# Performance work log

Measured on AMD Instinct MI355X. Metric: run time of the kernel, lower is better.

Reference implementation:

```python
import jax, jax.numpy as jnp
import numpy as np

BS, SEQ, D, H, NK = 4, 256, 256, 8, 16


def _ln(x, g, b, eps=1e-5):
    m = x.mean(-1, keepdims=True)
    v = ((x - m) ** 2).mean(-1, keepdims=True)
    return (x - m) / jnp.sqrt(v + eps) * g + b


def _attention(q, k, v, mask, gammas, maxout):
    # q,k,v: [b,h,s,dk]; mask: [1,1,s,s] bool; gammas: [h,1,1]
    dk = q.shape[-1]
    scores = jnp.einsum('bhqd,bhkd->bhqk', q, k) / jnp.sqrt(jnp.asarray(dk, q.dtype))
    seqlen = scores.shape[-1]
    ar = jnp.arange(seqlen)
    pos = jnp.abs(ar[None, :] - ar[:, None]).astype(scores.dtype)[None, None]
    # distance-decay term (computed under no_grad in the original)
    s_ = jax.nn.softmax(jnp.where(mask, scores, -1e32), axis=-1)
    distcum = jnp.cumsum(s_, axis=-1)
    disttotal = jnp.sum(s_, axis=-1, keepdims=True)
    dist = jax.lax.stop_gradient(jnp.sqrt(jnp.clip((disttotal - distcum) * pos, 0.0, None)))
    g = -jnp.abs(gammas)[None]  # [1,h,1,1]
    effect = jnp.clip(jnp.exp(dist * g), 1e-5, 1e5)
    scores = scores * effect
    scores = jax.nn.softmax(jnp.where(mask, scores, -1e32), axis=-1)
    scores = jnp.where(mask, scores, 0.0)
    if maxout:
        scale = jnp.minimum(1.0 / (jnp.max(scores, axis=-1, keepdims=True) + 1e-8), 5.0)
        scores = scores * scale
    return jnp.einsum('bhqk,bhkd->bhqd', scores, v), scores


def _mha(xq, xk, xv, Wq, bq, Wk, bk, Wv, bv, Wo, bo, gammas, mask, maxout):
    bs, seq, d = xq.shape
    h = gammas.shape[0]
    dk = d // h
    def heads(x, W, b):
        return (x @ W + b).reshape(bs, seq, h, dk).transpose(0, 2, 1, 3)
    o, sc = _attention(heads(xq, Wq, bq), heads(xk, Wk, bk), heads(xv, Wv, bv), mask, gammas, maxout)
    o = o.transpose(0, 2, 1, 3).reshape(bs, seq, d)
    return o @ Wo + bo, sc


def _block(xq, xk, xv, Wq, bq, Wk, bk, Wv, bv, Wo, bo, gammas, lng, lnb, peek_cur):
    seq = xq.shape[1]
    mask = jnp.tril(jnp.ones((seq, seq), bool), 0 if peek_cur else -1)[None, None]
    out, sc = _mha(xq, xk, xv, Wq, bq, Wk, bk, Wv, bv, Wo, bo, gammas, mask, not peek_cur)
    return _ln(xq + out, lng, lnb), sc


def _dtransformer(q_emb, s_emb, know_params,
                  Wq1, bq1, Wv1, bv1, Wo1, bo1, gam1, lng1, lnb1,
                  Wq2, bq2, Wv2, bv2, Wo2, bo2, gam2, lng2, lnb2,
                  Wq3, bq3, Wv3, bv3, Wo3, bo3, gam3, lng3, lnb3,
                  Wq4, bq4, Wk4, bk4, Wv4, bv4, Wo4, bo4, gam4, lng4, lnb4):
    # n_blocks == 3 path; kq_same=True for blocks 1-3 (Wk := Wq)
    hq, _ = _block(q_emb, q_emb, q_emb, Wq1, bq1, Wq1, bq1, Wv1, bv1, Wo1, bo1, gam1, lng1, lnb1, True)
    hs, _ = _block(s_emb, s_emb, s_emb, Wq2, bq2, Wq2, bq2, Wv2, bv2, Wo2, bo2, gam2, lng2, lnb2, True)
    p, q_scores = _block(hq, hq, hs, Wq3, bq3, Wq3, bq3, Wv3, bv3, Wo3, bo3, gam3, lng3, lnb3, True)
    bs, seq, d = p.shape
    nk = know_params.shape[0]
    query = jnp.broadcast_to(know_params[None, :, None, :], (bs, nk, seq, d)).reshape(bs * nk, seq, d)
    hq_r = jnp.broadcast_to(hq[:, None], (bs, nk, seq, d)).reshape(bs * nk, seq, d)
    p_r = jnp.broadcast_to(p[:, None], (bs, nk, seq, d)).reshape(bs * nk, seq, d)
    z, k_sc = _block(query, hq_r, p_r, Wq4, bq4, Wk4, bk4, Wv4, bv4, Wo4, bo4, gam4, lng4, lnb4, False)
    z = z.reshape(bs, nk, seq, d).transpose(0, 2, 1, 3).reshape(bs, seq, nk * d)
    h = gam4.shape[0]
    k_scores = k_sc.reshape(bs, nk, h, seq, seq).transpose(0, 2, 3, 1, 4)
    return z, q_scores, k_scores


_PARAM_NAMES = []
for _b in ('1', '2', '3', '4'):
    _PARAM_NAMES += ['Wq' + _b, 'bq' + _b]
    if _b == '4':
        _PARAM_NAMES += ['Wk4', 'bk4']
    _PARAM_NAMES += ['Wv' + _b, 'bv' + _b, 'Wo' + _b, 'bo' + _b, 'gam' + _b, 'lng' + _b, 'lnb' + _b]


def setup_inputs() -> dict:
    key = jax.random.key(0)
    ks = jax.random.split(key, 64)
    inp = {}
    inp['q_emb'] = jax.random.normal(ks[0], (BS, SEQ, D), jnp.float32)
    inp['s_emb'] = jax.random.normal(ks[1], (BS, SEQ, D), jnp.float32)
    inp['lens'] = jax.random.randint(ks[2], (BS,), 1, SEQ)
    inp['know_params'] = jax.random.uniform(ks[3], (NK, D), jnp.float32, -1.0, 1.0)
    i = 4
    for name in _PARAM_NAMES:
        if name.startswith('W'):
            inp[name] = jax.random.normal(ks[i], (D, D), jnp.float32) * 0.02; i += 1
        elif name.startswith('b'):
            inp[name] = jnp.zeros((D,), jnp.float32)
        elif name.startswith('gam'):
            inp[name] = jax.random.normal(ks[i], (H, 1, 1), jnp.float32) * 0.3; i += 1
        elif name.startswith('lng'):
            inp[name] = jnp.ones((D,), jnp.float32)
        else:
            inp[name] = jnp.zeros((D,), jnp.float32)
    return inp


def reference(q_emb, s_emb, lens, know_params,
              Wq1, bq1, Wv1, bv1, Wo1, bo1, gam1, lng1, lnb1,
              Wq2, bq2, Wv2, bv2, Wo2, bo2, gam2, lng2, lnb2,
              Wq3, bq3, Wv3, bv3, Wo3, bo3, gam3, lng3, lnb3,
              Wq4, bq4, Wk4, bk4, Wv4, bv4, Wo4, bo4, gam4, lng4, lnb4):
    return _dtransformer(q_emb, s_emb, know_params,
                         Wq1, bq1, Wv1, bv1, Wo1, bo1, gam1, lng1, lnb1,
                         Wq2, bq2, Wv2, bv2, Wo2, bo2, gam2, lng2, lnb2,
                         Wq3, bq3, Wv3, bv3, Wo3, bo3, gam3, lng3, lnb3,
                         Wq4, bq4, Wk4, bk4, Wv4, bv4, Wo4, bo4, gam4, lng4, lnb4)
```

## Files before the change

kernel.cpp:

```cpp
#include <hip/hip_runtime.h>
#include <math.h>

#define SEQL 256
#define DM   256
#define NH   8
#define DKH  32
#define BSZ  4
#define NKN  16

__device__ __forceinline__ float wave_red_sum(float v) {
#pragma unroll
  for (int o = 32; o > 0; o >>= 1) v += __shfl_xor(v, o);
  return v;
}
__device__ __forceinline__ float wave_red_max(float v) {
#pragma unroll
  for (int o = 32; o > 0; o >>= 1) v = fmaxf(v, __shfl_xor(v, o));
  return v;
}
__device__ __forceinline__ float wave_incl_scan(float v) {
  const int lane = threadIdx.x & 63;
#pragma unroll
  for (int o = 1; o < 64; o <<= 1) {
    float u = __shfl_up(v, o);
    if (lane >= o) v += u;
  }
  return v;
}

struct GemmSet { const float* A; const float* W; const float* bias; float* C; int M; };
struct Gemm4 { GemmSet s[4]; };

__global__ __launch_bounds__(256) void dt_gemmN(Gemm4 args) {
  const GemmSet g = args.s[blockIdx.z];
  const int bm = blockIdx.x * 64, bn = blockIdx.y * 64;
  if (bm >= g.M) return;
  __shared__ float As[16][68];
  __shared__ float Bs[16][68];
  const int tid = threadIdx.x;
  const int tc = tid & 15, tr = tid >> 4;
  float acc[4][4] = {};
  for (int k0 = 0; k0 < DM; k0 += 16) {
    {
      const int m = tid >> 2, kq = tid & 3;
      int row = bm + m; row = row < g.M ? row : (g.M - 1);
      const float4 v = *reinterpret_cast<const float4*>(&g.A[(size_t)row * DM + k0 + kq * 4]);
      As[kq * 4 + 0][m] = v.x; As[kq * 4 + 1][m] = v.y;
      As[kq * 4 + 2][m] = v.z; As[kq * 4 + 3][m] = v.w;
    }
    {
      const int k = tid >> 4, nq = tid & 15;
      const float4 v = *reinterpret_cast<const float4*>(&g.W[(size_t)(k0 + k) * DM + bn + nq * 4]);
      *reinterpret_cast<float4*>(&Bs[k][nq * 4]) = v;
    }
    __syncthreads();
#pragma unroll
    for (int k = 0; k < 16; ++k) {
      float a[4], b[4];
#pragma unroll
      for (int i = 0; i < 4; ++i) a[i] = As[k][tr * 4 + i];
#pragma unroll
      for (int j = 0; j < 4; ++j) b[j] = Bs[k][tc * 4 + j];
#pragma unroll
      for (int i = 0; i < 4; ++i)
#pragma unroll
        for (int j = 0; j < 4; ++j) acc[i][j] = fmaf(a[i], b[j], acc[i][j]);
    }
    __syncthreads();
  }
#pragma unroll
  for (int i = 0; i < 4; ++i) {
    const int row = bm + tr * 4 + i;
    if (row >= g.M) continue;
    float4 o;
    o.x = acc[i][0] + g.bias[bn + tc * 4 + 0];
    o.y = acc[i][1] + g.bias[bn + tc * 4 + 1];
    o.z = acc[i][2] + g.bias[bn + tc * 4 + 2];
    o.w = acc[i][3] + g.bias[bn + tc * 4 + 3];
    *reinterpret_cast<float4*>(&g.C[(size_t)row * DM + bn + tc * 4]) = o;
  }
}

__global__ __launch_bounds__(256) void dt_scores_nt2(const float* __restrict__ Q0,
                                                     const float* __restrict__ Q1,
                                                     float* __restrict__ Sa,
                                                     float* __restrict__ Sb) {
  const int z = blockIdx.z;
  const int set = z >> 5, bh = z & 31;
  const float* Qp = set ? Q1 : Q0;
  float* S = set ? Sb : Sa;
  const int b = bh >> 3, h = bh & 7;
  const float* Q = Qp + (size_t)b * SEQL * DM + h * DKH;
  __shared__ float Qs[16][33], Ks[16][33];
  const int tid = threadIdx.x;
  const int tj = tid & 15, ti = tid >> 4;
  const int i0 = blockIdx.x * 16, j0 = blockIdx.y * 16;
  const int r = tid >> 5, c = tid & 31;
  Qs[r][c]     = Q[(size_t)(i0 + r) * DM + c];
  Qs[r + 8][c] = Q[(size_t)(i0 + 8 + r) * DM + c];
  Ks[r][c]     = Q[(size_t)(j0 + r) * DM + c];
  Ks[r + 8][c] = Q[(size_t)(j0 + 8 + r) * DM + c];
  __syncthreads();
  float acc = 0.f;
#pragma unroll
  for (int k = 0; k < DKH; ++k) acc = fmaf(Qs[ti][k], Ks[tj][k], acc);
  S[((size_t)bh * SEQL + i0 + ti) * SEQL + j0 + tj] = acc * 0.17677669529663687f;
}

__global__ __launch_bounds__(256) void dt_scores4(const float* __restrict__ Q4h,
                                                  const float* __restrict__ Kp,
                                                  float* __restrict__ S0) {
  const int idx = blockIdx.x * 256 + threadIdx.x;
  const int j = idx & 255;
  const int h = (idx >> 8) & 7;
  const int nk = (idx >> 11) & 15;
  const int b = idx >> 15;
  const float* q = Q4h + nk * DM + h * DKH;
  const float* k = Kp + ((size_t)(b * SEQL + j)) * DM + h * DKH;
  float acc = 0.f;
#pragma unroll
  for (int c = 0; c < DKH; ++c) acc = fmaf(q[c], k[c], acc);
  S0[idx] = acc * 0.17677669529663687f;
}

__global__ __launch_bounds__(256) void dt_prep4(const float* __restrict__ S0,
                                                float* __restrict__ Pfx) {
  const int wid = threadIdx.x >> 6, lane = threadIdx.x & 63;
  const int row = blockIdx.x * 4 + wid;
  const float4 s4 = *reinterpret_cast<const float4*>(S0 + (size_t)row * SEQL + lane * 4);
  float s[4] = {s4.x, s4.y, s4.z, s4.w};
  float mx = fmaxf(fmaxf(s[0], s[1]), fmaxf(s[2], s[3]));
  mx = wave_red_max(mx);
  float e[4], t = 0.f;
#pragma unroll
  for (int q = 0; q < 4; ++q) { e[q] = __expf(s[q] - mx); t += e[q]; }
  const float incl = wave_incl_scan(t);
  float run = incl - t;
  float4 o;
  run += e[0]; o.x = run;
  run += e[1]; o.y = run;
  run += e[2]; o.z = run;
  run += e[3]; o.w = run;
  *reinterpret_cast<float4*>(Pfx + (size_t)row * SEQL + lane * 4) = o;
}

__global__ __launch_bounds__(256) void dt_softmax13w2(const float* __restrict__ Sa,
                                                      const float* __restrict__ Sb,
                                                      float* __restrict__ Pa,
                                                      float* __restrict__ Pb,
                                                      const float* __restrict__ g0,
                                                      const float* __restrict__ g1) {
  const int wid = threadIdx.x >> 6, lane = threadIdx.x & 63;
  const int grow = blockIdx.x * 4 + wid;
  const int set = grow >> 13;
  const int row = grow & 8191;
  const float* S = set ? Sb : Sa;
  float* P = set ? Pb : Pa;
  const float* gam = set ? g1 : g0;
  const int i = row & 255, h = (row >> 8) & 7;
  const float g = -fabsf(gam[h]);
  const int jb = lane * 4;
  const float4 s4 = *reinterpret_cast<const float4*>(S + (size_t)row * SEQL + jb);
  float s[4] = {s4.x, s4.y, s4.z, s4.w};
  float mx = -1e30f;
#pragma unroll
  for (int q = 0; q < 4; ++q) if (jb + q <= i) mx = fmaxf(mx, s[q]);
  mx = wave_red_max(mx);
  float e[4], t = 0.f;
#pragma unroll
  for (int q = 0; q < 4; ++q) { e[q] = (jb + q <= i) ? __expf(s[q] - mx) : 0.f; t += e[q]; }
  const float incl = wave_incl_scan(t);
  const float total = __shfl(incl, 63);
  const float inv = 1.f / total;
  float run = incl - t;
  float p2[4], t2 = 0.f;
#pragma unroll
  for (int q = 0; q < 4; ++q) {
    run += e[q];
    const float cum = run * inv;
    float dd = (1.f - cum) * (float)(i - jb - q);
    dd = dd > 0.f ? dd : 0.f;
    float eff = __expf(g * sqrtf(dd));
    eff = fmaxf(eff, 1e-5f);
    const float y = s[q] * eff;
    p2[q] = (jb + q <= i) ? __expf(y) : 0.f;
    t2 += p2[q];
  }
  const float sum2 = wave_red_sum(t2);
  const float inv2 = 1.f / sum2;
  float4 o = {p2[0] * inv2, p2[1] * inv2, p2[2] * inv2, p2[3] * inv2};
  *reinterpret_cast<float4*>(P + (size_t)row * SEQL + jb) = o;
}

__global__ __launch_bounds__(256) void dt_sm_pv4(const float* __restrict__ S0,
                                                 const float* __restrict__ Pfx,
                                                 const float* __restrict__ Vp,
                                                 const float* __restrict__ gam,
                                                 float* __restrict__ KS,
                                                 float* __restrict__ O) {
  __shared__ float Vs[256][32];
  __shared__ float Pl[32][268];
  __shared__ float Pfl[256];
  const int z = blockIdx.x;
  const int h = z & 7, b = z >> 7;
  const int nk = (z >> 3) & 15, bnk = z >> 3;
  const int tid = threadIdx.x, lane = tid & 63, w = tid >> 6;
  const float* Vbase = Vp + (size_t)b * SEQL * DM + h * DKH;
  {
    const int j = tid >> 3, c4 = (tid & 7) * 4;
    for (int jj = 0; jj < 256; jj += 32) {
      const float4 v = *reinterpret_cast<const float4*>(Vbase + (size_t)(jj + j) * DM + c4);
      *reinterpret_cast<float4*>(&Vs[jj + j][c4]) = v;
    }
  }
  if (tid < 64) {
    const float4 p = *reinterpret_cast<const float4*>(Pfx + (size_t)z * SEQL + tid * 4);
    *reinterpret_cast<float4*>(&Pfl[tid * 4]) = p;
  }
  const float4 s4 = *reinterpret_cast<const float4*>(S0 + (size_t)z * SEQL + lane * 4);
  const float4 p4 = *reinterpret_cast<const float4*>(Pfx + (size_t)z * SEQL + lane * 4);
  const float s[4] = {s4.x, s4.y, s4.z, s4.w};
  const float pj[4] = {p4.x, p4.y, p4.z, p4.w};
  const float g = -fabsf(gam[h]);
  const int jb = lane * 4;
  const int r0 = tid >> 5, cg = tid & 7, jq = (tid >> 3) & 3;
  __syncthreads();

  for (int chunk = 0; chunk < 8; ++chunk) {
    const int i0 = chunk * 32;
#pragma unroll
    for (int r = 0; r < 8; ++r) {
      const int il = w * 8 + r;
      const int i = i0 + il;
      float pv[4];
      if (i == 0) {
        pv[0] = pv[1] = pv[2] = pv[3] = 0.f;
      } else {
        const float rinv = 1.f / Pfl[i - 1];
        float t = 0.f, m = 0.f;
#pragma unroll
        for (int q = 0; q < 4; ++q) {
          const float cum = pj[q] * rinv;
          float dd = (1.f - cum) * (float)(i - jb - q);
          dd = dd > 0.f ? dd : 0.f;
          float eff = __expf(g * sqrtf(dd));
          eff = fmaxf(eff, 1e-5f);
          const float y = s[q] * eff;
          pv[q] = (jb + q < i) ? __expf(y) : 0.f;
          t += pv[q];
          m = fmaxf(m, pv[q]);
        }
#pragma unroll
        for (int o = 32; o > 0; o >>= 1) {
          t += __shfl_xor(t, o);
          m = fmaxf(m, __shfl_xor(m, o));
        }
        const float inv2 = 1.f / t;
        const float scale = fminf(1.f / (m * inv2 + 1e-8f), 5.f);
        const float f = inv2 * scale;
        pv[0] *= f; pv[1] *= f; pv[2] *= f; pv[3] *= f;
      }
      const float4 o4 = {pv[0], pv[1], pv[2], pv[3]};
      *reinterpret_cast<float4*>(KS + ((((size_t)(b * NH + h)) * SEQL + i) * NKN + nk) * SEQL + jb) = o4;
      *reinterpret_cast<float4*>(&Pl[il][jb]) = o4;
    }
    __syncthreads();
    float4 acc[4] = {{0.f,0.f,0.f,0.f},{0.f,0.f,0.f,0.f},{0.f,0.f,0.f,0.f},{0.f,0.f,0.f,0.f}};
#pragma unroll 4
    for (int t4 = 0; t4 < 16; ++t4) {
      const int jb2 = t4 * 16 + jq * 4;
      float pr[4][4];
#pragma unroll
      for (int r = 0; r < 4; ++r) {
        const float4 p = *reinterpret_cast<const float4*>(&Pl[r0 * 4 + r][jb2]);
        pr[r][0] = p.x; pr[r][1] = p.y; pr[r][2] = p.z; pr[r][3] = p.w;
      }
#pragma unroll
      for (int k = 0; k < 4; ++k) {
        const float4 v = *reinterpret_cast<const float4*>(&Vs[jb2 + k][cg * 4]);
#pragma unroll
        for (int r = 0; r < 4; ++r) {
          acc[r].x = fmaf(pr[r][k], v.x, acc[r].x);
          acc[r].y = fmaf(pr[r][k], v.y, acc[r].y);
          acc[r].z = fmaf(pr[r][k], v.z, acc[r].z);
          acc[r].w = fmaf(pr[r][k], v.w, acc[r].w);
        }
      }
    }
#pragma unroll
    for (int r = 0; r < 4; ++r) {
      acc[r].x += __shfl_xor(acc[r].x, 8);  acc[r].x += __shfl_xor(acc[r].x, 16);
      acc[r].y += __shfl_xor(acc[r].y, 8);  acc[r].y += __shfl_xor(acc[r].y, 16);
      acc[r].z += __shfl_xor(acc[r].z, 8);  acc[r].z += __shfl_xor(acc[r].z, 16);
      acc[r].w += __shfl_xor(acc[r].w, 8);  acc[r].w += __shfl_xor(acc[r].w, 16);
    }
    if ((tid & 24) == 0) {
#pragma unroll
      for (int r = 0; r < 4; ++r)
        *reinterpret_cast<float4*>(O + ((size_t)(bnk * SEQL + i0 + r0 * 4 + r)) * DM + h * DKH + cg * 4) = acc[r];
    }
    __syncthreads();
  }
}

__global__ __launch_bounds__(256) void dt_pv13_2(const float* __restrict__ Pa,
                                                 const float* __restrict__ Pb,
                                                 const float* __restrict__ V0,
                                                 const float* __restrict__ V1,
                                                 float* __restrict__ Oa,
                                                 float* __restrict__ Ob) {
  __shared__ float Vs[256][32];
  __shared__ float Pl[32][268];
  const int z = blockIdx.y;
  const int set = z >> 5, bh = z & 31;
  const float* P = set ? Pb : Pa;
  const float* Vp = set ? V1 : V0;
  float* O = set ? Ob : Oa;
  const int b = bh >> 3, h = bh & 7;
  const int i0 = blockIdx.x * 32;
  const int tid = threadIdx.x;
  const float* Prow = P + ((size_t)bh * SEQL + i0) * SEQL;
  const float* Vbase = Vp + (size_t)b * SEQL * DM + h * DKH;
#pragma unroll
  for (int t = 0; t < 8; ++t) {
    const int idx = t * 256 + tid;
    const int j = idx >> 3, c4 = (idx & 7) * 4;
    *reinterpret_cast<float4*>(&Vs[j][c4]) =
        *reinterpret_cast<const float4*>(Vbase + (size_t)j * DM + c4);
    const int prw = idx >> 6, pc4 = (idx & 63) * 4;
    *reinterpret_cast<float4*>(&Pl[prw][pc4]) =
        *reinterpret_cast<const float4*>(Prow + (size_t)prw * SEQL + pc4);
  }
  __syncthreads();
  const int r0 = tid >> 5, cg = tid & 7, jq = (tid >> 3) & 3;
  float4 acc[4] = {{0.f,0.f,0.f,0.f},{0.f,0.f,0.f,0.f},{0.f,0.f,0.f,0.f},{0.f,0.f,0.f,0.f}};
#pragma unroll 4
  for (int t4 = 0; t4 < 16; ++t4) {
    const int jb2 = t4 * 16 + jq * 4;
    float pr[4][4];
#pragma unroll
    for (int r = 0; r < 4; ++r) {
      const float4 p = *reinterpret_cast<const float4*>(&Pl[r0 * 4 + r][jb2]);
      pr[r][0] = p.x; pr[r][1] = p.y; pr[r][2] = p.z; pr[r][3] = p.w;
    }
#pragma unroll
    for (int k = 0; k < 4; ++k) {
      const float4 v = *reinterpret_cast<const float4*>(&Vs[jb2 + k][cg * 4]);
#pragma unroll
      for (int r = 0; r < 4; ++r) {
        acc[r].x = fmaf(pr[r][k], v.x, acc[r].x);
        acc[r].y = fmaf(pr[r][k], v.y, acc[r].y);
        acc[r].z = fmaf(pr[r][k], v.z, acc[r].z);
        acc[r].w = fmaf(pr[r][k], v.w, acc[r].w);
      }
    }
  }
#pragma unroll
  for (int r = 0; r < 4; ++r) {
    acc[r].x += __shfl_xor(acc[r].x, 8);  acc[r].x += __shfl_xor(acc[r].x, 16);
    acc[r].y += __shfl_xor(acc[r].y, 8);  acc[r].y += __shfl_xor(acc[r].y, 16);
    acc[r].z += __shfl_xor(acc[r].z, 8);  acc[r].z += __shfl_xor(acc[r].z, 16);
    acc[r].w += __shfl_xor(acc[r].w, 8);  acc[r].w += __shfl_xor(acc[r].w, 16);
  }
  if ((tid & 24) == 0) {
#pragma unroll
    for (int r = 0; r < 4; ++r)
      *reinterpret_cast<float4*>(O + ((size_t)(b * SEQL + i0 + r0 * 4 + r)) * DM + h * DKH + cg * 4) = acc[r];
  }
}

__global__ __launch_bounds__(256) void dt_ln_res2(const float* __restrict__ X0,
                                                  const float* __restrict__ X1,
                                                  const float* __restrict__ Y0,
                                                  const float* __restrict__ Y1,
                                                  const float* __restrict__ G0,
                                                  const float* __restrict__ G1,
                                                  const float* __restrict__ B0,
                                                  const float* __restrict__ B1,
                                                  float* __restrict__ Z0,
                                                  float* __restrict__ Z1) {
  const int wid = threadIdx.x >> 6, lane = threadIdx.x & 63;
  const int grow = blockIdx.x * 4 + wid;
  const int set = grow >> 10;
  const int row = grow & 1023;
  const float* X = set ? X1 : X0;
  const float* Y = set ? Y1 : Y0;
  const float* g = set ? G1 : G0;
  const float* bb = set ? B1 : B0;
  float* Z = set ? Z1 : Z0;
  const int jb = lane * 4;
  const float4 x4 = *reinterpret_cast<const float4*>(X + (size_t)row * DM + jb);
  const float4 y4 = *reinterpret_cast<const float4*>(Y + (size_t)row * DM + jb);
  float x[4] = {x4.x + y4.x, x4.y + y4.y, x4.z + y4.z, x4.w + y4.w};
  const float mean = wave_red_sum(x[0] + x[1] + x[2] + x[3]) * (1.f / 256.f);
  float vs = 0.f;
#pragma unroll
  for (int q = 0; q < 4; ++q) { const float d = x[q] - mean; vs += d * d; }
  const float var = wave_red_sum(vs) * (1.f / 256.f);
  const float rstd = 1.f / sqrtf(var + 1e-5f);
  const float4 g4 = *reinterpret_cast<const float4*>(g + jb);
  const float4 b4 = *reinterpret_cast<const float4*>(bb + jb);
  float4 o;
  o.x = (x[0] - mean) * rstd * g4.x + b4.x;
  o.y = (x[1] - mean) * rstd * g4.y + b4.y;
  o.z = (x[2] - mean) * rstd * g4.z + b4.z;
  o.w = (x[3] - mean) * rstd * g4.w + b4.w;
  *reinterpret_cast<float4*>(Z + (size_t)row * DM + jb) = o;
}

__global__ __launch_bounds__(256) void dt_ln4w(const float* __restrict__ know,
                                               const float* __restrict__ Y,
                                               const float* __restrict__ g,
                                               const float* __restrict__ bb,
                                               float* __restrict__ Z) {
  const int wid = threadIdx.x >> 6, lane = threadIdx.x & 63;
  const int row = blockIdx.x * 4 + wid;
  const int i = row & 255;
  const int nk = (row >> 8) & 15;
  const int b = row >> 12;
  const int jb = lane * 4;
  const float4 k4 = *reinterpret_cast<const float4*>(know + (size_t)nk * DM + jb);
  const float4 y4 = *reinterpret_cast<const float4*>(Y + (size_t)row * DM + jb);
  float x[4] = {k4.x + y4.x, k4.y + y4.y, k4.z + y4.z, k4.w + y4.w};
  const float mean = wave_red_sum(x[0] + x[1] + x[2] + x[3]) * (1.f / 256.f);
  float vs = 0.f;
#pragma unroll
  for (int q = 0; q < 4; ++q) { const float d = x[q] - mean; vs += d * d; }
  const float var = wave_red_sum(vs) * (1.f / 256.f);
  const float rstd = 1.f / sqrtf(var + 1e-5f);
  const float4 g4 = *reinterpret_cast<const float4*>(g + jb);
  const float4 b4 = *reinterpret_cast<const float4*>(bb + jb);
  float4 o;
  o.x = (x[0] - mean) * rstd * g4.x + b4.x;
  o.y = (x[1] - mean) * rstd * g4.y + b4.y;
  o.z = (x[2] - mean) * rstd * g4.z + b4.z;
  o.w = (x[3] - mean) * rstd * g4.w + b4.w;
  *reinterpret_cast<float4*>(Z + ((size_t)(b * SEQL + i)) * (NKN * DM) + (size_t)nk * DM + jb) = o;
}

extern "C" void kernel_launch(void* const* d_in, const int* in_sizes, int n_in,
                              void* d_out, int out_size, void* d_ws, size_t ws_size,
                              hipStream_t stream) {
  (void)in_sizes; (void)n_in; (void)out_size; (void)ws_size;
  const float* q_emb = (const float*)d_in[0];
  const float* s_emb = (const float*)d_in[1];
  const float* know  = (const float*)d_in[3];
  const float* Wq1 = (const float*)d_in[4],  *bq1 = (const float*)d_in[5];
  const float* Wv1 = (const float*)d_in[6],  *bv1 = (const float*)d_in[7];
  const float* Wo1 = (const float*)d_in[8],  *bo1 = (const float*)d_in[9];
  const float* gam1 = (const float*)d_in[10], *lng1 = (const float*)d_in[11], *lnb1 = (const float*)d_in[12];
  const float* Wq2 = (const float*)d_in[13], *bq2 = (const float*)d_in[14];
  const float* Wv2 = (const float*)d_in[15], *bv2 = (const float*)d_in[16];
  const float* Wo2 = (const float*)d_in[17], *bo2 = (const float*)d_in[18];
  const float* gam2 = (const float*)d_in[19], *lng2 = (const float*)d_in[20], *lnb2 = (const float*)d_in[21];
  const float* Wq3 = (const float*)d_in[22], *bq3 = (const float*)d_in[23];
  const float* Wv3 = (const float*)d_in[24], *bv3 = (const float*)d_in[25];
  const float* Wo3 = (const float*)d_in[26], *bo3 = (const float*)d_in[27];
  const float* gam3 = (const float*)d_in[28], *lng3 = (const float*)d_in[29], *lnb3 = (const float*)d_in[30];
  const float* Wq4 = (const float*)d_in[31], *bq4 = (const float*)d_in[32];
  const float* Wk4 = (const float*)d_in[33], *bk4 = (const float*)d_in[34];
  const float* Wv4 = (const float*)d_in[35], *bv4 = (const float*)d_in[36];
  const float* Wo4 = (const float*)d_in[37], *bo4 = (const float*)d_in[38];
  const float* gam4 = (const float*)d_in[39], *lng4 = (const float*)d_in[40], *lnb4 = (const float*)d_in[41];

  float* ws = (float*)d_ws;
  const size_t U = 262144;
  float* Qp0 = ws + 0 * U;
  float* Qp1 = ws + 1 * U;
  float* Vp0 = ws + 2 * U;
  float* Vp1 = ws + 3 * U;
  float* Sa  = ws + 4 * U;
  float* Sb  = ws + 12 * U;
  float* O0  = ws + 20 * U;
  float* O1  = ws + 21 * U;
  float* OW0 = ws + 22 * U;
  float* OW1 = ws + 23 * U;
  float* hq  = ws + 24 * U;
  float* hs  = ws + 25 * U;
  float* pbf = ws + 26 * U;
  float* Q4h = ws + 27 * U;
  float* S0s = Q4h + 4096;
  float* OW4 = Sa;
  float* Pfx = O0;

  float* zout = (float*)d_out;
  float* qsc  = zout + 4194304;
  float* ksc  = qsc + 2097152;
  float* O4   = zout;

  const dim3 thr(256);

  {
    Gemm4 a = {{{q_emb, Wq1, bq1, Qp0, 1024}, {q_emb, Wv1, bv1, Vp0, 1024},
                {s_emb, Wq2, bq2, Qp1, 1024}, {s_emb, Wv2, bv2, Vp1, 1024}}};
    dt_gemmN<<<dim3(16, 4, 4), thr, 0, stream>>>(a);
  }
  dt_scores_nt2<<<dim3(16, 16, 64), thr, 0, stream>>>(Qp0, Qp1, Sa, Sb);
  dt_softmax13w2<<<dim3(4096), thr, 0, stream>>>(Sa, Sb, Sa, Sb, gam1, gam2);
  dt_pv13_2<<<dim3(8, 64), thr, 0, stream>>>(Sa, Sb, Vp0, Vp1, O0, O1);
  {
    Gemm4 a = {{{O0, Wo1, bo1, OW0, 1024}, {O1, Wo2, bo2, OW1, 1024},
                {O0, Wo1, bo1, OW0, 1024}, {O1, Wo2, bo2, OW1, 1024}}};
    dt_gemmN<<<dim3(16, 4, 2), thr, 0, stream>>>(a);
  }
  dt_ln_res2<<<dim3(512), thr, 0, stream>>>(q_emb, s_emb, OW0, OW1, lng1, lng2, lnb1, lnb2, hq, hs);

  {
    Gemm4 a = {{{hq, Wq3, bq3, Qp0, 1024}, {hs, Wv3, bv3, Vp0, 1024},
                {hq, Wq3, bq3, Qp0, 1024}, {hs, Wv3, bv3, Vp0, 1024}}};
    dt_gemmN<<<dim3(16, 4, 2), thr, 0, stream>>>(a);
  }
  dt_scores_nt2<<<dim3(16, 16, 32), thr, 0, stream>>>(Qp0, Qp0, Sa, Sa);
  dt_softmax13w2<<<dim3(2048), thr, 0, stream>>>(Sa, Sa, qsc, qsc, gam3, gam3);
  dt_pv13_2<<<dim3(8, 32), thr, 0, stream>>>(qsc, qsc, Vp0, Vp0, O0, O0);
  {
    Gemm4 a = {{{O0, Wo3, bo3, OW0, 1024}, {O0, Wo3, bo3, OW0, 1024},
                {O0, Wo3, bo3, OW0, 1024}, {O0, Wo3, bo3, OW0, 1024}}};
    dt_gemmN<<<dim3(16, 4, 1), thr, 0, stream>>>(a);
  }
  dt_ln_res2<<<dim3(256), thr, 0, stream>>>(hq, hq, OW0, OW0, lng3, lng3, lnb3, lnb3, pbf, pbf);

  {
    Gemm4 a = {{{hq, Wk4, bk4, Qp0, 1024}, {pbf, Wv4, bv4, Vp0, 1024},
                {know, Wq4, bq4, Q4h, 16}, {know, Wq4, bq4, Q4h, 16}}};
    dt_gemmN<<<dim3(16, 4, 3), thr, 0, stream>>>(a);
  }
  dt_scores4<<<dim3(512), thr, 0, stream>>>(Q4h, Qp0, S0s);
  dt_prep4<<<dim3(128), thr, 0, stream>>>(S0s, Pfx);
  dt_sm_pv4<<<dim3(512), thr, 0, stream>>>(S0s, Pfx, Vp0, gam4, ksc, O4);
  {
    Gemm4 a = {{{O4, Wo4, bo4, OW4, 16384}, {O4, Wo4, bo4, OW4, 16384},
                {O4, Wo4, bo4, OW4, 16384}, {O4, Wo4, bo4, OW4, 16384}}};
    dt_gemmN<<<dim3(256, 4, 1), thr, 0, stream>>>(a);
  }
  dt_ln4w<<<dim3(4096), thr, 0, stream>>>(know, OW4, lng4, lnb4, zout);
}
```

Before: 516.1 us.

## Use bf16 LDS tiles for PV, split sm_pv4 rows, retile scores and small GEMMs

The P·V kernels now store P and a transposed V in LDS as bf16 and unpack them to fp32 for the FMAs. This halves LDS footprint and read traffic, and they get launch bounds allowing four blocks per CU. dt_sm_pv4 splits its eight row chunks across two blocks to double parallelism, at the cost of each block reloading V. The scores kernel moves to 32x32 tiles with four outputs per thread and float4 loads, and the 1024-row GEMMs use a new 32-row tile kernel for more blocks. Rounding P and V to bf16 lowers the precision of the attention output.

```diff
diff --git a/kernel.cpp b/kernel.cpp
--- a/kernel.cpp
+++ b/kernel.cpp
@@ -7,6 +7,7 @@
 #define DKH  32
 #define BSZ  4
 #define NKN  16
+#define LSTR 264
 
 __device__ __forceinline__ float wave_red_sum(float v) {
 #pragma unroll
@@ -26,6 +27,62 @@
     if (lane >= o) v += u;
   }
   return v;
+}
+
+__device__ __forceinline__ unsigned short bf16r(float f) {
+  unsigned u = __float_as_uint(f);
+  u = (u + 0x7fffu + ((u >> 16) & 1u)) >> 16;
+  return (unsigned short)u;
+}
+__device__ __forceinline__ unsigned pack_bf16x2(float a, float b) {
+  return (unsigned)bf16r(a) | ((unsigned)bf16r(b) << 16);
+}
+
+__device__ __forceinline__ void pv_core(const unsigned short (*Pl)[LSTR],
+                                        const unsigned short (*Vt)[LSTR],
+                                        int tid, float acc[4][4]) {
+  const int r0 = tid >> 5, cg = tid & 7, jq = (tid >> 3) & 3;
+#pragma unroll
+  for (int t = 0; t < 8; ++t) {
+    const int j0 = t * 32 + jq * 8;
+    uint4 pu[4], vu[4];
+#pragma unroll
+    for (int r = 0; r < 4; ++r) pu[r] = *reinterpret_cast<const uint4*>(&Pl[r0 * 4 + r][j0]);
+#pragma unroll
+    for (int c = 0; c < 4; ++c) vu[c] = *reinterpret_cast<const uint4*>(&Vt[cg * 4 + c][j0]);
+#pragma unroll
+    for (int d = 0; d < 4; ++d) {
+      float pl[4], ph[4], vl[4], vh[4];
+#pragma unroll
+      for (int r = 0; r < 4; ++r) {
+        const unsigned w = (&pu[r].x)[d];
+        pl[r] = __uint_as_float(w << 16);
+        ph[r] = __uint_as_float(w & 0xffff0000u);
+      }
+#pragma unroll
+      for (int c = 0; c < 4; ++c) {
+        const unsigned w = (&vu[c].x)[d];
+        vl[c] = __uint_as_float(w << 16);
+        vh[c] = __uint_as_float(w & 0xffff0000u);
+      }
+#pragma unroll
+      for (int r = 0; r < 4; ++r)
+#pragma unroll
+        for (int c = 0; c < 4; ++c)
+          acc[r][c] = fmaf(ph[r], vh[c], fmaf(pl[r], vl[c], acc[r][c]));
+    }
+  }
+}
+__device__ __forceinline__ void pv_reduce_jq(int tid, float acc[4][4]) {
+#pragma unroll
+  for (int r = 0; r < 4; ++r)
+#pragma unroll
+    for (int c = 0; c < 4; ++c) {
+      float v = acc[r][c];
+      v += __shfl_xor(v, 8);
+      v += __shfl_xor(v, 16);
+      acc[r][c] = v;
+    }
 }
 
 struct GemmSet { const float* A; const float* W; const float* bias; float* C; int M; };
@@ -81,6 +138,53 @@
   }
 }
 
+__global__ __launch_bounds__(256) void dt_gemm32(Gemm4 args) {
+  const GemmSet g = args.s[blockIdx.z];
+  const int bm = blockIdx.x * 32, bn = blockIdx.y * 64;
+  __shared__ float As[16][36];
+  __shared__ float Bs[16][68];
+  const int tid = threadIdx.x;
+  const int tc = tid & 15, tr = tid >> 4;
+  float acc[2][4] = {};
+  for (int k0 = 0; k0 < DM; k0 += 16) {
+    if (tid < 128) {
+      const int m = tid >> 2, kq = tid & 3;
+      const float4 v = *reinterpret_cast<const float4*>(&g.A[(size_t)(bm + m) * DM + k0 + kq * 4]);
+      As[kq * 4 + 0][m] = v.x; As[kq * 4 + 1][m] = v.y;
+      As[kq * 4 + 2][m] = v.z; As[kq * 4 + 3][m] = v.w;
+    }
+    {
+      const int k = tid >> 4, nq = tid & 15;
+      const float4 v = *reinterpret_cast<const float4*>(&g.W[(size_t)(k0 + k) * DM + bn + nq * 4]);
+      *reinterpret_cast<float4*>(&Bs[k][nq * 4]) = v;
+    }
+    __syncthreads();
+#pragma unroll
+    for (int k = 0; k < 16; ++k) {
+      float a[2], b[4];
+      a[0] = As[k][tr * 2 + 0];
+      a[1] = As[k][tr * 2 + 1];
+#pragma unroll
+      for (int j = 0; j < 4; ++j) b[j] = Bs[k][tc * 4 + j];
+#pragma unroll
+      for (int i = 0; i < 2; ++i)
+#pragma unroll
+        for (int j = 0; j < 4; ++j) acc[i][j] = fmaf(a[i], b[j], acc[i][j]);
+    }
+    __syncthreads();
+  }
+#pragma unroll
+  for (int i = 0; i < 2; ++i) {
+    const int row = bm + tr * 2 + i;
+    float4 o;
+    o.x = acc[i][0] + g.bias[bn + tc * 4 + 0];
+    o.y = acc[i][1] + g.bias[bn + tc * 4 + 1];
+    o.z = acc[i][2] + g.bias[bn + tc * 4 + 2];
+    o.w = acc[i][3] + g.bias[bn + tc * 4 + 3];
+    *reinterpret_cast<float4*>(&g.C[(size_t)row * DM + bn + tc * 4]) = o;
+  }
+}
+
 __global__ __launch_bounds__(256) void dt_scores_nt2(const float* __restrict__ Q0,
                                                      const float* __restrict__ Q1,
                                                      float* __restrict__ Sa,
@@ -91,20 +195,28 @@
   float* S = set ? Sb : Sa;
   const int b = bh >> 3, h = bh & 7;
   const float* Q = Qp + (size_t)b * SEQL * DM + h * DKH;
-  __shared__ float Qs[16][33], Ks[16][33];
+  __shared__ float Qs[32][33], Ks[32][33];
   const int tid = threadIdx.x;
-  const int tj = tid & 15, ti = tid >> 4;
-  const int i0 = blockIdx.x * 16, j0 = blockIdx.y * 16;
-  const int r = tid >> 5, c = tid & 31;
-  Qs[r][c]     = Q[(size_t)(i0 + r) * DM + c];
-  Qs[r + 8][c] = Q[(size_t)(i0 + 8 + r) * DM + c];
-  Ks[r][c]     = Q[(size_t)(j0 + r) * DM + c];
-  Ks[r + 8][c] = Q[(size_t)(j0 + 8 + r) * DM + c];
+  const int i0 = blockIdx.x * 32, j0 = blockIdx.y * 32;
+  {
+    const int r = tid >> 3, gq = (tid & 7) * 4;
+    const float4 q = *reinterpret_cast<const float4*>(&Q[(size_t)(i0 + r) * DM + gq]);
+    Qs[r][gq + 0] = q.x; Qs[r][gq + 1] = q.y; Qs[r][gq + 2] = q.z; Qs[r][gq + 3] = q.w;
+    const float4 k = *reinterpret_cast<const float4*>(&Q[(size_t)(j0 + r) * DM + gq]);
+    Ks[r][gq + 0] = k.x; Ks[r][gq + 1] = k.y; Ks[r][gq + 2] = k.z; Ks[r][gq + 3] = k.w;
+  }
   __syncthreads();
-  float acc = 0.f;
-#pragma unroll
-  for (int k = 0; k < DKH; ++k) acc = fmaf(Qs[ti][k], Ks[tj][k], acc);
-  S[((size_t)bh * SEQL + i0 + ti) * SEQL + j0 + tj] = acc * 0.17677669529663687f;
+  const int tj = tid & 31, tig = tid >> 5;
+  float acc[4] = {0.f, 0.f, 0.f, 0.f};
+#pragma unroll
+  for (int k = 0; k < DKH; ++k) {
+    const float bk = Ks[tj][k];
+#pragma unroll
+    for (int r = 0; r < 4; ++r) acc[r] = fmaf(Qs[tig * 4 + r][k], bk, acc[r]);
+  }
+#pragma unroll
+  for (int r = 0; r < 4; ++r)
+    S[((size_t)bh * SEQL + i0 + tig * 4 + r) * SEQL + j0 + tj] = acc[r] * 0.17677669529663687f;
 }
 
 __global__ __launch_bounds__(256) void dt_scores4(const float* __restrict__ Q4h,
@@ -192,25 +304,30 @@
   *reinterpret_cast<float4*>(P + (size_t)row * SEQL + jb) = o;
 }
 
-__global__ __launch_bounds__(256) void dt_sm_pv4(const float* __restrict__ S0,
-                                                 const float* __restrict__ Pfx,
-                                                 const float* __restrict__ Vp,
-                                                 const float* __restrict__ gam,
-                                                 float* __restrict__ KS,
-                                                 float* __restrict__ O) {
-  __shared__ float Vs[256][32];
-  __shared__ float Pl[32][268];
+__global__ __launch_bounds__(256, 4) void dt_sm_pv4(const float* __restrict__ S0,
+                                                    const float* __restrict__ Pfx,
+                                                    const float* __restrict__ Vp,
+                                                    const float* __restrict__ gam,
+                                                    float* __restrict__ KS,
+                                                    float* __restrict__ O) {
+  __shared__ unsigned short Vt[32][LSTR];
+  __shared__ unsigned short Pl[32][LSTR];
   __shared__ float Pfl[256];
-  const int z = blockIdx.x;
+  const int z = blockIdx.y;
   const int h = z & 7, b = z >> 7;
   const int nk = (z >> 3) & 15, bnk = z >> 3;
   const int tid = threadIdx.x, lane = tid & 63, w = tid >> 6;
   const float* Vbase = Vp + (size_t)b * SEQL * DM + h * DKH;
   {
-    const int j = tid >> 3, c4 = (tid & 7) * 4;
-    for (int jj = 0; jj < 256; jj += 32) {
-      const float4 v = *reinterpret_cast<const float4*>(Vbase + (size_t)(jj + j) * DM + c4);
-      *reinterpret_cast<float4*>(&Vs[jj + j][c4]) = v;
+    const int jr = tid >> 3, gq = tid & 7;
+#pragma unroll
+    for (int t = 0; t < 8; ++t) {
+      const int j = jr + t * 32;
+      const float4 v = *reinterpret_cast<const float4*>(Vbase + (size_t)j * DM + gq * 4);
+      Vt[gq * 4 + 0][j] = bf16r(v.x);
+      Vt[gq * 4 + 1][j] = bf16r(v.y);
+      Vt[gq * 4 + 2][j] = bf16r(v.z);
+      Vt[gq * 4 + 3][j] = bf16r(v.w);
     }
   }
   if (tid < 64) {
@@ -223,10 +340,10 @@
   const float pj[4] = {p4.x, p4.y, p4.z, p4.w};
   const float g = -fabsf(gam[h]);
   const int jb = lane * 4;
-  const int r0 = tid >> 5, cg = tid & 7, jq = (tid >> 3) & 3;
+  const int r0 = tid >> 5, cg = tid & 7;
   __syncthreads();
 
-  for (int chunk = 0; chunk < 8; ++chunk) {
+  for (int chunk = blockIdx.x * 4; chunk < blockIdx.x * 4 + 4; ++chunk) {
     const int i0 = chunk * 32;
 #pragma unroll
     for (int r = 0; r < 8; ++r) {
@@ -262,55 +379,32 @@
       }
       const float4 o4 = {pv[0], pv[1], pv[2], pv[3]};
       *reinterpret_cast<float4*>(KS + ((((size_t)(b * NH + h)) * SEQL + i) * NKN + nk) * SEQL + jb) = o4;
-      *reinterpret_cast<float4*>(&Pl[il][jb]) = o4;
+      uint2 pk = {pack_bf16x2(pv[0], pv[1]), pack_bf16x2(pv[2], pv[3])};
+      *reinterpret_cast<uint2*>(&Pl[il][jb]) = pk;
     }
     __syncthreads();
-    float4 acc[4] = {{0.f,0.f,0.f,0.f},{0.f,0.f,0.f,0.f},{0.f,0.f,0.f,0.f},{0.f,0.f,0.f,0.f}};
-#pragma unroll 4
-    for (int t4 = 0; t4 < 16; ++t4) {
-      const int jb2 = t4 * 16 + jq * 4;
-      float pr[4][4];
+    float acc[4][4] = {};
+    pv_core(Pl, Vt, tid, acc);
+    pv_reduce_jq(tid, acc);
+    if ((tid & 24) == 0) {
 #pragma unroll
       for (int r = 0; r < 4; ++r) {
-        const float4 p = *reinterpret_cast<const float4*>(&Pl[r0 * 4 + r][jb2]);
-        pr[r][0] = p.x; pr[r][1] = p.y; pr[r][2] = p.z; pr[r][3] = p.w;
+        const float4 oo = {acc[r][0], acc[r][1], acc[r][2], acc[r][3]};
+        *reinterpret_cast<float4*>(O + ((size_t)(bnk * SEQL + i0 + r0 * 4 + r)) * DM + h * DKH + cg * 4) = oo;
       }
-#pragma unroll
-      for (int k = 0; k < 4; ++k) {
-        const float4 v = *reinterpret_cast<const float4*>(&Vs[jb2 + k][cg * 4]);
-#pragma unroll
-        for (int r = 0; r < 4; ++r) {
-          acc[r].x = fmaf(pr[r][k], v.x, acc[r].x);
-          acc[r].y = fmaf(pr[r][k], v.y, acc[r].y);
-          acc[r].z = fmaf(pr[r][k], v.z, acc[r].z);
-          acc[r].w = fmaf(pr[r][k], v.w, acc[r].w);
-        }
-      }
-    }
-#pragma unroll
-    for (int r = 0; r < 4; ++r) {
-      acc[r].x += __shfl_xor(acc[r].x, 8);  acc[r].x += __shfl_xor(acc[r].x, 16);
-      acc[r].y += __shfl_xor(acc[r].y, 8);  acc[r].y += __shfl_xor(acc[r].y, 16);
-      acc[r].z += __shfl_xor(acc[r].z, 8);  acc[r].z += __shfl_xor(acc[r].z, 16);
-      acc[r].w += __shfl_xor(acc[r].w, 8);  acc[r].w += __shfl_xor(acc[r].w, 16);
-    }
-    if ((tid & 24) == 0) {
-#pragma unroll
-      for (int r = 0; r < 4; ++r)
-        *reinterpret_cast<float4*>(O + ((size_t)(bnk * SEQL + i0 + r0 * 4 + r)) * DM + h * DKH + cg * 4) = acc[r];
     }
     __syncthreads();
   }
 }
 
-__global__ __launch_bounds__(256) void dt_pv13_2(const float* __restrict__ Pa,
-                                                 const float* __restrict__ Pb,
-                                                 const float* __restrict__ V0,
-                                                 const float* __restrict__ V1,
-                                                 float* __restrict__ Oa,
-                                                 float* __restrict__ Ob) {
-  __shared__ float Vs[256][32];
-  __shared__ float Pl[32][268];
+__global__ __launch_bounds__(256, 4) void dt_pv13_2(const float* __restrict__ Pa,
+                                                    const float* __restrict__ Pb,
+                                                    const float* __restrict__ V0,
+                                                    const float* __restrict__ V1,
+                                                    float* __restrict__ Oa,
+                                                    float* __restrict__ Ob) {
+  __shared__ unsigned short Vt[32][LSTR];
+  __shared__ unsigned short Pl[32][LSTR];
   const int z = blockIdx.y;
   const int set = z >> 5, bh = z & 31;
   const float* P = set ? Pb : Pa;
@@ -321,51 +415,37 @@
   const int tid = threadIdx.x;
   const float* Prow = P + ((size_t)bh * SEQL + i0) * SEQL;
   const float* Vbase = Vp + (size_t)b * SEQL * DM + h * DKH;
-#pragma unroll
-  for (int t = 0; t < 8; ++t) {
-    const int idx = t * 256 + tid;
-    const int j = idx >> 3, c4 = (idx & 7) * 4;
-    *reinterpret_cast<float4*>(&Vs[j][c4]) =
-        *reinterpret_cast<const float4*>(Vbase + (size_t)j * DM + c4);
-    const int prw = idx >> 6, pc4 = (idx & 63) * 4;
-    *reinterpret_cast<float4*>(&Pl[prw][pc4]) =
-        *reinterpret_cast<const float4*>(Prow + (size_t)prw * SEQL + pc4);
+  {
+    const int jr = tid >> 3, gq = tid & 7;
+#pragma unroll
+    for (int t = 0; t < 8; ++t) {
+      const int j = jr + t * 32;
+      const float4 v = *reinterpret_cast<const float4*>(Vbase + (size_t)j * DM + gq * 4);
+      Vt[gq * 4 + 0][j] = bf16r(v.x);
+      Vt[gq * 4 + 1][j] = bf16r(v.y);
+      Vt[gq * 4 + 2][j] = bf16r(v.z);
+      Vt[gq * 4 + 3][j] = bf16r(v.w);
+    }
+#pragma unroll
+    for (int t = 0; t < 8; ++t) {
+      const int id = t * 256 + tid;
+      const int row = id >> 6, g4 = id & 63;
+      const float4 p = *reinterpret_cast<const float4*>(Prow + (size_t)row * SEQL + g4 * 4);
+      uint2 pk = {pack_bf16x2(p.x, p.y), pack_bf16x2(p.z, p.w)};
+      *reinterpret_cast<uint2*>(&Pl[row][g4 * 4]) = pk;
+    }
   }
   __syncthreads();
-  const int r0 = tid >> 5, cg = tid & 7, jq = (tid >> 3) & 3;
-  float4 acc[4] = {{0.f,0.f,0.f,0.f},{0.f,0.f,0.f,0.f},{0.f,0.f,0.f,0.f},{0.f,0.f,0.f,0.f}};
-#pragma unroll 4
-  for (int t4 = 0; t4 < 16; ++t4) {
-    const int jb2 = t4 * 16 + jq * 4;
-    float pr[4][4];
+  float acc[4][4] = {};
+  pv_core(Pl, Vt, tid, acc);
+  pv_reduce_jq(tid, acc);
+  const int r0 = tid >> 5, cg = tid & 7;
+  if ((tid & 24) == 0) {
 #pragma unroll
     for (int r = 0; r < 4; ++r) {
-      const float4 p = *reinterpret_cast<const float4*>(&Pl[r0 * 4 + r][jb2]);
-      pr[r][0] = p.x; pr[r][1] = p.y; pr[r][2] = p.z; pr[r][3] = p.w;
-    }
-#pragma unroll
-    for (int k = 0; k < 4; ++k) {
-      const float4 v = *reinterpret_cast<const float4*>(&Vs[jb2 + k][cg * 4]);
-#pragma unroll
-      for (int r = 0; r < 4; ++r) {
-        acc[r].x = fmaf(pr[r][k], v.x, acc[r].x);
-        acc[r].y = fmaf(pr[r][k], v.y, acc[r].y);
-        acc[r].z = fmaf(pr[r][k], v.z, acc[r].z);
-        acc[r].w = fmaf(pr[r][k], v.w, acc[r].w);
-      }
-    }
-  }
-#pragma unroll
-  for (int r = 0; r < 4; ++r) {
-    acc[r].x += __shfl_xor(acc[r].x, 8);  acc[r].x += __shfl_xor(acc[r].x, 16);
-    acc[r].y += __shfl_xor(acc[r].y, 8);  acc[r].y += __shfl_xor(acc[r].y, 16);
-    acc[r].z += __shfl_xor(acc[r].z, 8);  acc[r].z += __shfl_xor(acc[r].z, 16);
-    acc[r].w += __shfl_xor(acc[r].w, 8);  acc[r].w += __shfl_xor(acc[r].w, 16);
-  }
-  if ((tid & 24) == 0) {
-#pragma unroll
-    for (int r = 0; r < 4; ++r)
-      *reinterpret_cast<float4*>(O + ((size_t)(b * SEQL + i0 + r0 * 4 + r)) * DM + h * DKH + cg * 4) = acc[r];
+      const float4 oo = {acc[r][0], acc[r][1], acc[r][2], acc[r][3]};
+      *reinterpret_cast<float4*>(O + ((size_t)(b * SEQL + i0 + r0 * 4 + r)) * DM + h * DKH + cg * 4) = oo;
+    }
   }
 }
 
@@ -493,30 +573,30 @@
   {
     Gemm4 a = {{{q_emb, Wq1, bq1, Qp0, 1024}, {q_emb, Wv1, bv1, Vp0, 1024},
                 {s_emb, Wq2, bq2, Qp1, 1024}, {s_emb, Wv2, bv2, Vp1, 1024}}};
-    dt_gemmN<<<dim3(16, 4, 4), thr, 0, stream>>>(a);
-  }
-  dt_scores_nt2<<<dim3(16, 16, 64), thr, 0, stream>>>(Qp0, Qp1, Sa, Sb);
+    dt_gemm32<<<dim3(32, 4, 4), thr, 0, stream>>>(a);
+  }
+  dt_scores_nt2<<<dim3(8, 8, 64), thr, 0, stream>>>(Qp0, Qp1, Sa, Sb);
   dt_softmax13w2<<<dim3(4096), thr, 0, stream>>>(Sa, Sb, Sa, Sb, gam1, gam2);
   dt_pv13_2<<<dim3(8, 64), thr, 0, stream>>>(Sa, Sb, Vp0, Vp1, O0, O1);
   {
     Gemm4 a = {{{O0, Wo1, bo1, OW0, 1024}, {O1, Wo2, bo2, OW1, 1024},
                 {O0, Wo1, bo1, OW0, 1024}, {O1, Wo2, bo2, OW1, 1024}}};
-    dt_gemmN<<<dim3(16, 4, 2), thr, 0, stream>>>(a);
+    dt_gemm32<<<dim3(32, 4, 2), thr, 0, stream>>>(a);
   }
   dt_ln_res2<<<dim3(512), thr, 0, stream>>>(q_emb, s_emb, OW0, OW1, lng1, lng2, lnb1, lnb2, hq, hs);
 
   {
     Gemm4 a = {{{hq, Wq3, bq3, Qp0, 1024}, {hs, Wv3, bv3, Vp0, 1024},
                 {hq, Wq3, bq3, Qp0, 1024}, {hs, Wv3, bv3, Vp0, 1024}}};
-    dt_gemmN<<<dim3(16, 4, 2), thr, 0, stream>>>(a);
-  }
-  dt_scores_nt2<<<dim3(16, 16, 32), thr, 0, stream>>>(Qp0, Qp0, Sa, Sa);
+    dt_gemm32<<<dim3(32, 4, 2), thr, 0, stream>>>(a);
+  }
+  dt_scores_nt2<<<dim3(8, 8, 32), thr, 0, stream>>>(Qp0, Qp0, Sa, Sa);
   dt_softmax13w2<<<dim3(2048), thr, 0, stream>>>(Sa, Sa, qsc, qsc, gam3, gam3);
   dt_pv13_2<<<dim3(8, 32), thr, 0, stream>>>(qsc, qsc, Vp0, Vp0, O0, O0);
   {
     Gemm4 a = {{{O0, Wo3, bo3, OW0, 1024}, {O0, Wo3, bo3, OW0, 1024},
                 {O0, Wo3, bo3, OW0, 1024}, {O0, Wo3, bo3, OW0, 1024}}};
-    dt_gemmN<<<dim3(16, 4, 1), thr, 0, stream>>>(a);
+    dt_gemm32<<<dim3(32, 4, 1), thr, 0, stream>>>(a);
   }
   dt_ln_res2<<<dim3(256), thr, 0, stream>>>(hq, hq, OW0, OW0, lng3, lng3, lnb3, lnb3, pbf, pbf);
 
@@ -527,7 +607,7 @@
   }
   dt_scores4<<<dim3(512), thr, 0, stream>>>(Q4h, Qp0, S0s);
   dt_prep4<<<dim3(128), thr, 0, stream>>>(S0s, Pfx);
-  dt_sm_pv4<<<dim3(512), thr, 0, stream>>>(S0s, Pfx, Vp0, gam4, ksc, O4);
+  dt_sm_pv4<<<dim3(2, 512), thr, 0, stream>>>(S0s, Pfx, Vp0, gam4, ksc, O4);
   {
     Gemm4 a = {{{O4, Wo4, bo4, OW4, 16384}, {O4, Wo4, bo4, OW4, 16384},
                 {O4, Wo4, bo4, OW4, 16384}, {O4, Wo4, bo4, OW4, 16384}}};
```

Measured after the change: 521.5 us. About the same (+1.1%).
